# Kernel optimization log

Hardware: AMD Instinct MI355X
Metric: run time of the kernel (lower is better)

## Reference

```python
import jax, jax.numpy as jnp
import numpy as np

# dims: batch, seq, d_model, heads, head_dim, ffn, layers, vocab, group_size
B, S, D, H, DH, DFF, L, V, GS = 2, 1024, 1024, 16, 64, 4096, 2, 32000, 128
EPS = 1e-6


def _dequant(t, s):
    # t: int8 ternary codes [out, in]; s: per-group scales [out*in//GS]
    return (t.reshape(-1, GS).astype(jnp.float32) * s[:, None]).reshape(t.shape)


def _rmsnorm(x, w):
    return x * jax.lax.rsqrt(jnp.mean(x * x, axis=-1, keepdims=True) + EPS) * w


def setup_inputs() -> dict:
    key = jax.random.key(0)
    ks = iter(jax.random.split(key, 64))

    def tern(shape):
        return jax.random.randint(next(ks), shape, -1, 2).astype(jnp.int8)

    def sc(n):
        return jax.random.uniform(next(ks), (n,), minval=0.01, maxval=0.05, dtype=jnp.float32)

    ng_dd = D * D // GS
    ng_fd = DFF * D // GS
    ng_vd = V * D // GS
    inp = {
        'input_ids': jax.random.randint(next(ks), (B, S), 0, V, dtype=jnp.int32),
        'emb_t': tern((V, D)), 'emb_s': sc(ng_vd),
        'qt': tern((L, D, D)), 'qs': jnp.stack([sc(ng_dd) for _ in range(L)]),
        'kt': tern((L, D, D)), 'ks_': jnp.stack([sc(ng_dd) for _ in range(L)]),
        'vt': tern((L, D, D)), 'vs': jnp.stack([sc(ng_dd) for _ in range(L)]),
        'ot': tern((L, D, D)), 'os_': jnp.stack([sc(ng_dd) for _ in range(L)]),
        'gatet': tern((L, DFF, D)), 'gates': jnp.stack([sc(ng_fd) for _ in range(L)]),
        'upt': tern((L, DFF, D)), 'ups': jnp.stack([sc(ng_fd) for _ in range(L)]),
        'downt': tern((L, D, DFF)), 'downs': jnp.stack([sc(ng_fd) for _ in range(L)]),
        'wa': jnp.ones((L, D), jnp.float32),
        'wm': jnp.ones((L, D), jnp.float32),
        'alpha': jnp.full((L, H, 1, 1), 0.5, jnp.float32),
        'wf': jnp.ones((D,), jnp.float32),
        'headt': tern((V, D)), 'heads_': sc(ng_vd),
    }
    return inp


def reference(input_ids, emb_t, emb_s, qt, qs, kt, ks_, vt, vs, ot, os_,
              gatet, gates, upt, ups, downt, downs, wa, wm, alpha, wf,
              headt, heads_):
    # ternary embedding: dequant full table then gather (matches F.embedding on reconstructed weight)
    x = _dequant(emb_t, emb_s)[input_ids]                 # [B, S, D]
    causal = jnp.tril(jnp.ones((S, S), bool))             # [S, S]
    scale = DH ** -0.5
    for l in range(L):
        # --- attention block ---
        h = _rmsnorm(x, wa[l])
        Wq, Wk, Wv, Wo = (_dequant(qt[l], qs[l]), _dequant(kt[l], ks_[l]),
                          _dequant(vt[l], vs[l]), _dequant(ot[l], os_[l]))
        q = (h @ Wq.T).reshape(B, S, H, DH).transpose(0, 2, 1, 3)
        k = (h @ Wk.T).reshape(B, S, H, DH).transpose(0, 2, 1, 3)
        v = (h @ Wv.T).reshape(B, S, H, DH).transpose(0, 2, 1, 3)
        attn = jnp.einsum('bhsd,bhtd->bhst', q, k) * scale
        attn = jnp.where(causal, attn, -jnp.inf)
        p = jax.nn.softmax(attn, axis=-1)
        o = jnp.einsum('bhst,bhtd->bhsd', p, v)
        # per-head residual: alpha * input heads (input to attention is the normed h)
        h_heads = h.reshape(B, S, H, DH).transpose(0, 2, 1, 3)
        o = o + alpha[l] * h_heads
        o = o.transpose(0, 2, 1, 3).reshape(B, S, D)
        x = x + o @ Wo.T
        # --- SwiGLU MLP block ---
        hm = _rmsnorm(x, wm[l])
        Wg, Wu, Wd = (_dequant(gatet[l], gates[l]), _dequant(upt[l], ups[l]),
                      _dequant(downt[l], downs[l]))
        x = x + (jax.nn.silu(hm @ Wg.T) * (hm @ Wu.T)) @ Wd.T
    x = _rmsnorm(x, wf)
    logits = x @ _dequant(headt, heads_).T                # [B, S, V]
    return logits
```

## Files before the change

### kernel.cpp

```cpp
#include <hip/hip_runtime.h>
#include <math.h>
#include <stdint.h>

#define BB   2
#define SS   1024
#define DD   1024
#define HH   16
#define DHH  64
#define DFFD 4096
#define LL   2
#define VV   32000
#define GSZ  128
#define BSR  (BB*SS)
constexpr float EPS = 1e-6f;

typedef unsigned short ushort_t;
typedef __bf16 bf16x8 __attribute__((ext_vector_type(8)));
typedef short  short8 __attribute__((ext_vector_type(8)));
typedef unsigned short ushort8v __attribute__((ext_vector_type(8)));
typedef float  f32x4  __attribute__((ext_vector_type(4)));

__device__ inline ushort_t f2bf(float f) {
    unsigned int u = __builtin_bit_cast(unsigned int, f);
    unsigned int r = u + 0x7fffu + ((u >> 16) & 1u);
    return (ushort_t)(r >> 16);
}
__device__ inline float bf2f(ushort_t u) {
    unsigned int x = ((unsigned int)u) << 16;
    return __builtin_bit_cast(float, x);
}

#define GL2L(g, l) __builtin_amdgcn_global_load_lds( \
    (const __attribute__((address_space(1))) void*)(g), \
    (__attribute__((address_space(3))) void*)(l), 16, 0, 0)

__global__ __launch_bounds__(256) void k_dequant(const int* __restrict__ T,
                                                 const float* __restrict__ S,
                                                 ushort_t* __restrict__ W) {
    int i = (blockIdx.x * 256 + threadIdx.x) * 4;
    int4 t = *(const int4*)(T + i);
    float s = S[i >> 7];
    ushort4 w;
    w.x = f2bf((float)t.x * s); w.y = f2bf((float)t.y * s);
    w.z = f2bf((float)t.z * s); w.w = f2bf((float)t.w * s);
    *(ushort4*)(W + i) = w;
}

__global__ __launch_bounds__(256) void k_embed(const int* __restrict__ ids,
                                               const int* __restrict__ t,
                                               const float* __restrict__ s,
                                               float* __restrict__ x) {
    int row = blockIdx.x;
    int id  = ids[row];
    for (int d = threadIdx.x; d < DD; d += 256) {
        x[(size_t)row * DD + d] =
            (float)t[(size_t)id * DD + d] * s[id * (DD / GSZ) + (d >> 7)];
    }
}

__global__ __launch_bounds__(256) void k_rmsnorm(const float* __restrict__ x,
                                                 const float* __restrict__ w,
                                                 ushort_t* __restrict__ o) {
    int row = blockIdx.x;
    const float* xr = x + (size_t)row * DD;
    float ss = 0.f;
    for (int d = threadIdx.x; d < DD; d += 256) { float v = xr[d]; ss += v * v; }
    __shared__ float sm[4];
    for (int off = 32; off > 0; off >>= 1) ss += __shfl_down(ss, off, 64);
    if ((threadIdx.x & 63) == 0) sm[threadIdx.x >> 6] = ss;
    __syncthreads();
    float tot = sm[0] + sm[1] + sm[2] + sm[3];
    float inv = rsqrtf(tot / DD + EPS);
    for (int d = threadIdx.x; d < DD; d += 256)
        o[(size_t)row * DD + d] = f2bf(xr[d] * inv * w[d]);
}

template <int MODE>
__global__ __launch_bounds__(256) void gemm_bf16(const ushort_t* __restrict__ A,
                                                 const ushort_t* __restrict__ W,
                                                 float* __restrict__ Cf,
                                                 ushort_t* __restrict__ Cb,
                                                 const float* __restrict__ Gf,
                                                 int M, int N, int K) {
    __shared__ ushort_t As[128 * 32];
    __shared__ ushort_t Bs[128 * 32];
    const int tid  = threadIdx.x;
    const int wave = tid >> 6, lane = tid & 63;
    const int wm = wave >> 1, wn = wave & 1;
    const int i0 = blockIdx.y * 128, o0 = blockIdx.x * 128;

    f32x4 acc[4][4] = {};

    const int srow = wave * 32 + (lane >> 2);
    const int scol = (lane & 3) * 8;
    const ushort_t* aG0 = A + (size_t)(i0 + srow) * K + scol;
    const ushort_t* aG1 = aG0 + (size_t)16 * K;
    const ushort_t* bG0 = W + (size_t)(o0 + srow) * K + scol;
    const ushort_t* bG1 = bG0 + (size_t)16 * K;
    ushort_t* aL0 = As + wave * 1024;
    ushort_t* aL1 = aL0 + 512;
    ushort_t* bL0 = Bs + wave * 1024;
    ushort_t* bL1 = bL0 + 512;

    const ushort_t* ap = As + (wm * 64 + (lane & 15)) * 32 + (lane >> 4) * 8;
    const ushort_t* bp = Bs + (wn * 64 + (lane & 15)) * 32 + (lane >> 4) * 8;

    for (int k0 = 0; k0 < K; k0 += 32) {
        __syncthreads();
        GL2L(aG0 + k0, aL0);
        GL2L(aG1 + k0, aL1);
        GL2L(bG0 + k0, bL0);
        GL2L(bG1 + k0, bL1);
        __syncthreads();
        bf16x8 av[4], bv[4];
#pragma unroll
        for (int t = 0; t < 4; ++t) {
            av[t] = __builtin_bit_cast(bf16x8, *(const short8*)(ap + t * 512));
            bv[t] = __builtin_bit_cast(bf16x8, *(const short8*)(bp + t * 512));
        }
#pragma unroll
        for (int mt = 0; mt < 4; ++mt)
#pragma unroll
            for (int nt = 0; nt < 4; ++nt)
                acc[mt][nt] = __builtin_amdgcn_mfma_f32_16x16x32_bf16(
                    av[mt], bv[nt], acc[mt][nt], 0, 0, 0);
    }

    const int r0 = wm * 64 + (lane >> 4) * 4;
    const int c0 = wn * 64 + (lane & 15);
#pragma unroll
    for (int mt = 0; mt < 4; ++mt) {
#pragma unroll
        for (int r = 0; r < 4; ++r) {
            const size_t row = i0 + r0 + mt * 16 + r;
#pragma unroll
            for (int nt = 0; nt < 4; ++nt) {
                const size_t col = o0 + c0 + nt * 16;
                const size_t idx = row * (size_t)N + col;
                float v = acc[mt][nt][r];
                if (MODE == 0) {
                    Cf[idx] = v;
                } else if (MODE == 1) {
                    Cf[idx] += v;
                } else if (MODE == 2) {
                    float gv = Gf[idx];
                    Cb[idx] = f2bf(gv / (1.f + __expf(-gv)) * v);
                } else {
                    Cb[idx] = f2bf(v);
                }
            }
        }
    }
}

__global__ __launch_bounds__(256) void k_fattn(const ushort_t* __restrict__ qkv,
                                               const ushort_t* __restrict__ hn,
                                               const float* __restrict__ alpha,
                                               ushort_t* __restrict__ out) {
    __shared__ ushort_t Ks[64][72];
    __shared__ ushort_t Vt[64][72];
    __shared__ ushort_t Ps[4][16][72];

    const int bid = blockIdx.x;
    const int bh  = bid & 31;
    const int qt  = 15 - (bid >> 5);
    const int hh  = bh & 15;
    const int b   = bh >> 4;
    const int tid = threadIdx.x;
    const int wm  = tid >> 6;
    const int ln  = tid & 63;
    const int m16 = ln & 15;
    const int q4  = ln >> 4;

    const int bS0 = b * SS;
    const int q0  = qt * 64 + wm * 16;

    bf16x8 qa0, qa1;
    {
        const ushort_t* qp = qkv + (size_t)(bS0 + q0 + m16) * 3072 + hh * DHH + q4 * 8;
        qa0 = __builtin_bit_cast(bf16x8, *(const ushort8v*)(qp));
        qa1 = __builtin_bit_cast(bf16x8, *(const ushort8v*)(qp + 32));
    }

    f32x4 oacc[4] = {};
    float mrow[4] = {-1e30f, -1e30f, -1e30f, -1e30f};
    float lrow[4] = {0.f, 0.f, 0.f, 0.f};

    const int c0a = tid, c1a = tid + 256;
    const int r0a = c0a >> 3, cc0 = (c0a & 7) * 8;
    const int r1a = c1a >> 3, cc1 = (c1a & 7) * 8;

    for (int t = 0; t <= qt; ++t) {
        __syncthreads();
        {
            const size_t kbase = (size_t)(bS0 + t * 64) * 3072 + 1024 + hh * DHH;
            *(ushort8v*)&Ks[r0a][cc0] = *(const ushort8v*)(qkv + kbase + (size_t)r0a * 3072 + cc0);
            *(ushort8v*)&Ks[r1a][cc1] = *(const ushort8v*)(qkv + kbase + (size_t)r1a * 3072 + cc1);
            const size_t vbase = (size_t)(bS0 + t * 64) * 3072 + 2048 + hh * DHH;
            ushort8v v0 = *(const ushort8v*)(qkv + vbase + (size_t)r0a * 3072 + cc0);
#pragma unroll
            for (int j = 0; j < 8; ++j) Vt[cc0 + j][r0a] = v0[j];
            ushort8v v1 = *(const ushort8v*)(qkv + vbase + (size_t)r1a * 3072 + cc1);
#pragma unroll
            for (int j = 0; j < 8; ++j) Vt[cc1 + j][r1a] = v1[j];
        }
        __syncthreads();

        f32x4 sc[4];
#pragma unroll
        for (int nt = 0; nt < 4; ++nt) {
            bf16x8 kb0 = __builtin_bit_cast(bf16x8, *(const ushort8v*)&Ks[nt * 16 + m16][q4 * 8]);
            bf16x8 kb1 = __builtin_bit_cast(bf16x8, *(const ushort8v*)&Ks[nt * 16 + m16][32 + q4 * 8]);
            f32x4 z = {};
            z = __builtin_amdgcn_mfma_f32_16x16x32_bf16(qa0, kb0, z, 0, 0, 0);
            sc[nt] = __builtin_amdgcn_mfma_f32_16x16x32_bf16(qa1, kb1, z, 0, 0, 0);
        }

        const bool diag = (t == qt);
#pragma unroll
        for (int r = 0; r < 4; ++r) {
            float s0 = sc[0][r] * 0.125f;
            float s1 = sc[1][r] * 0.125f;
            float s2 = sc[2][r] * 0.125f;
            float s3 = sc[3][r] * 0.125f;
            if (diag) {
                const int rl = wm * 16 + q4 * 4 + r;
                if (m16      > rl) s0 = -1e30f;
                if (m16 + 16 > rl) s1 = -1e30f;
                if (m16 + 32 > rl) s2 = -1e30f;
                if (m16 + 48 > rl) s3 = -1e30f;
            }
            float tm = fmaxf(fmaxf(s0, s1), fmaxf(s2, s3));
            tm = fmaxf(tm, __shfl_xor(tm, 1, 64));
            tm = fmaxf(tm, __shfl_xor(tm, 2, 64));
            tm = fmaxf(tm, __shfl_xor(tm, 4, 64));
            tm = fmaxf(tm, __shfl_xor(tm, 8, 64));
            const float mnew = fmaxf(mrow[r], tm);
            const float corr = __expf(mrow[r] - mnew);
            const float e0 = __expf(s0 - mnew);
            const float e1 = __expf(s1 - mnew);
            const float e2 = __expf(s2 - mnew);
            const float e3 = __expf(s3 - mnew);
            float rs = e0 + e1 + e2 + e3;
            rs += __shfl_xor(rs, 1, 64);
            rs += __shfl_xor(rs, 2, 64);
            rs += __shfl_xor(rs, 4, 64);
            rs += __shfl_xor(rs, 8, 64);
            lrow[r] = lrow[r] * corr + rs;
            mrow[r] = mnew;
#pragma unroll
            for (int dt = 0; dt < 4; ++dt) oacc[dt][r] *= corr;
            const int pr = q4 * 4 + r;
            Ps[wm][pr][m16]      = f2bf(e0);
            Ps[wm][pr][m16 + 16] = f2bf(e1);
            Ps[wm][pr][m16 + 32] = f2bf(e2);
            Ps[wm][pr][m16 + 48] = f2bf(e3);
        }

#pragma unroll
        for (int ks = 0; ks < 2; ++ks) {
            bf16x8 pa = __builtin_bit_cast(bf16x8, *(const ushort8v*)&Ps[wm][m16][ks * 32 + q4 * 8]);
#pragma unroll
            for (int dt = 0; dt < 4; ++dt) {
                bf16x8 vb = __builtin_bit_cast(bf16x8, *(const ushort8v*)&Vt[dt * 16 + m16][ks * 32 + q4 * 8]);
                oacc[dt] = __builtin_amdgcn_mfma_f32_16x16x32_bf16(pa, vb, oacc[dt], 0, 0, 0);
            }
        }
    }

    const float al = alpha[hh];
#pragma unroll
    for (int r = 0; r < 4; ++r) {
        const float inv = 1.f / lrow[r];
        const size_t row = (size_t)(bS0 + q0 + q4 * 4 + r);
#pragma unroll
        for (int dt = 0; dt < 4; ++dt) {
            const size_t idx = row * DD + hh * DHH + dt * 16 + m16;
            out[idx] = f2bf(oacc[dt][r] * inv + al * bf2f(hn[idx]));
        }
    }
}

extern "C" void kernel_launch(void* const* d_in, const int* in_sizes, int n_in,
                              void* d_out, int out_size, void* d_ws, size_t ws_size,
                              hipStream_t stream) {
    const int*   ids   = (const int*)d_in[0];
    const int*   emb_t = (const int*)d_in[1];
    const float* emb_s = (const float*)d_in[2];
    const int*   qt    = (const int*)d_in[3];
    const float* qs    = (const float*)d_in[4];
    const int*   kt    = (const int*)d_in[5];
    const float* ks    = (const float*)d_in[6];
    const int*   vt    = (const int*)d_in[7];
    const float* vs    = (const float*)d_in[8];
    const int*   ot    = (const int*)d_in[9];
    const float* os    = (const float*)d_in[10];
    const int*   gatet = (const int*)d_in[11];
    const float* gates = (const float*)d_in[12];
    const int*   upt   = (const int*)d_in[13];
    const float* ups   = (const float*)d_in[14];
    const int*   downt = (const int*)d_in[15];
    const float* downs = (const float*)d_in[16];
    const float* wa    = (const float*)d_in[17];
    const float* wm    = (const float*)d_in[18];
    const float* alpha = (const float*)d_in[19];
    const float* wf    = (const float*)d_in[20];
    const int*   headt = (const int*)d_in[21];
    const float* heads = (const float*)d_in[22];

    const size_t MB = 1ull << 20;
    char* wsb = (char*)d_ws;
    ushort_t* wbuf = (ushort_t*)(wsb);
    float*    g    = (float*)   (wsb + 24 * MB);
    ushort_t* gb   = (ushort_t*)(wsb + 58 * MB);
    float*    x    = (float*)   (wsb + 75 * MB);
    ushort_t* h    = (ushort_t*)(wsb + 84 * MB);
    ushort_t* qkvb = (ushort_t*)(wsb + 89 * MB);
    ushort_t* ao   = (ushort_t*)(wsb + 102 * MB);

    const size_t wDD = (size_t)DD * DD;
    const size_t sDD = wDD / GSZ;
    const size_t wFD = (size_t)DFFD * DD;
    const size_t sFD = wFD / GSZ;

    k_embed<<<BSR, 256, 0, stream>>>(ids, emb_t, emb_s, x);

    const dim3 gQKV(3072 / 128, BSR / 128);
    const dim3 gD(DD / 128, BSR / 128);
    const dim3 gF(DFFD / 128, BSR / 128);
    const dim3 gV(VV / 128, BSR / 128);

    for (int l = 0; l < LL; ++l) {
        k_rmsnorm<<<BSR, 256, 0, stream>>>(x, wa + l * DD, h);
        k_dequant<<<wDD / 1024, 256, 0, stream>>>(qt + l * wDD, qs + l * sDD, wbuf);
        k_dequant<<<wDD / 1024, 256, 0, stream>>>(kt + l * wDD, ks + l * sDD, wbuf + wDD);
        k_dequant<<<wDD / 1024, 256, 0, stream>>>(vt + l * wDD, vs + l * sDD, wbuf + 2 * wDD);
        gemm_bf16<3><<<gQKV, 256, 0, stream>>>(h, wbuf, nullptr, qkvb, nullptr, BSR, 3072, DD);
        k_fattn<<<16 * BB * HH, 256, 0, stream>>>(qkvb, h, alpha + l * HH, ao);
        k_dequant<<<wDD / 1024, 256, 0, stream>>>(ot + l * wDD, os + l * sDD, wbuf);
        gemm_bf16<1><<<gD, 256, 0, stream>>>(ao, wbuf, x, nullptr, nullptr, BSR, DD, DD);

        k_rmsnorm<<<BSR, 256, 0, stream>>>(x, wm + l * DD, h);
        k_dequant<<<wFD / 1024, 256, 0, stream>>>(gatet + l * wFD, gates + l * sFD, wbuf);
        gemm_bf16<0><<<gF, 256, 0, stream>>>(h, wbuf, g, nullptr, nullptr, BSR, DFFD, DD);
        k_dequant<<<wFD / 1024, 256, 0, stream>>>(upt + l * wFD, ups + l * sFD, wbuf);
        gemm_bf16<2><<<gF, 256, 0, stream>>>(h, wbuf, nullptr, gb, g, BSR, DFFD, DD);
        k_dequant<<<wFD / 1024, 256, 0, stream>>>(downt + l * wFD, downs + l * sFD, wbuf);
        gemm_bf16<1><<<gD, 256, 0, stream>>>(gb, wbuf, x, nullptr, nullptr, BSR, DD, DFFD);
    }

    k_rmsnorm<<<BSR, 256, 0, stream>>>(x, wf, h);
    k_dequant<<<((size_t)VV * DD) / 1024, 256, 0, stream>>>(headt, heads, wbuf);
    gemm_bf16<0><<<gV, 256, 0, stream>>>(h, wbuf, (float*)d_out, nullptr, nullptr, BSR, VV, DD);
}
```

Before: 1.255 ms.

## Fuse gate/up GEMMs via interleaved weights and remap workgroups for XCD locality

Gate and up weights are dequantized into a row-interleaved buffer so that a single GEMM with N=8192 computes both. Adjacent output columns are paired with a lane shuffle and the SwiGLU is applied in the epilogue. This removes the fp32 gate intermediate buffer, one GEMM launch, and the re-read of the activations. All GEMMs also move to a 1D grid with a workgroup remap that groups consecutive blocks on the same XCD, meant to improve L2 reuse. The remap hardcodes 16 M-tiles and needs the block count to be divisible by 8.

Result: faster. 1.217 ms (-3.0%).

```diff
diff --git a/kernel.cpp b/kernel.cpp
--- a/kernel.cpp
+++ b/kernel.cpp
@@ -44,6 +44,20 @@
     w.x = f2bf((float)t.x * s); w.y = f2bf((float)t.y * s);
     w.z = f2bf((float)t.z * s); w.w = f2bf((float)t.w * s);
     *(ushort4*)(W + i) = w;
+}
+
+__global__ __launch_bounds__(256) void k_dequant_il(const int* __restrict__ T,
+                                                    const float* __restrict__ S,
+                                                    ushort_t* __restrict__ W,
+                                                    int which) {
+    int i = (blockIdx.x * 256 + threadIdx.x) * 4;
+    int4 t = *(const int4*)(T + i);
+    float s = S[i >> 7];
+    ushort4 w;
+    w.x = f2bf((float)t.x * s); w.y = f2bf((float)t.y * s);
+    w.z = f2bf((float)t.z * s); w.w = f2bf((float)t.w * s);
+    int r = i >> 10, c = i & 1023;
+    *(ushort4*)(W + (((size_t)((r << 1) | which)) << 10) + c) = w;
 }
 
 __global__ __launch_bounds__(256) void k_embed(const int* __restrict__ ids,
@@ -80,14 +94,18 @@
                                                  const ushort_t* __restrict__ W,
                                                  float* __restrict__ Cf,
                                                  ushort_t* __restrict__ Cb,
-                                                 const float* __restrict__ Gf,
                                                  int M, int N, int K) {
     __shared__ ushort_t As[128 * 32];
     __shared__ ushort_t Bs[128 * 32];
     const int tid  = threadIdx.x;
     const int wave = tid >> 6, lane = tid & 63;
     const int wm = wave >> 1, wn = wave & 1;
-    const int i0 = blockIdx.y * 128, o0 = blockIdx.x * 128;
+
+    const int nwg  = gridDim.x;
+    const int orig = blockIdx.x;
+    const int wgid = (orig & 7) * (nwg >> 3) + (orig >> 3);
+    const int i0 = (wgid & 15) * 128;
+    const int o0 = (wgid >> 4) * 128;
 
     f32x4 acc[4][4] = {};
 
@@ -142,11 +160,15 @@
                     Cf[idx] = v;
                 } else if (MODE == 1) {
                     Cf[idx] += v;
-                } else if (MODE == 2) {
-                    float gv = Gf[idx];
-                    Cb[idx] = f2bf(gv / (1.f + __expf(-gv)) * v);
+                } else if (MODE == 3) {
+                    Cb[idx] = f2bf(v);
                 } else {
-                    Cb[idx] = f2bf(v);
+                    float pv = __shfl_xor(v, 1, 64);
+                    if (!(lane & 1)) {
+                        float g = v, u = pv;
+                        float res = g / (1.f + __expf(-g)) * u;
+                        Cb[row * (size_t)(N >> 1) + (col >> 1)] = f2bf(res);
+                    }
                 }
             }
         }
@@ -311,7 +333,6 @@
     const size_t MB = 1ull << 20;
     char* wsb = (char*)d_ws;
     ushort_t* wbuf = (ushort_t*)(wsb);
-    float*    g    = (float*)   (wsb + 24 * MB);
     ushort_t* gb   = (ushort_t*)(wsb + 58 * MB);
     float*    x    = (float*)   (wsb + 75 * MB);
     ushort_t* h    = (ushort_t*)(wsb + 84 * MB);
@@ -325,31 +346,25 @@
 
     k_embed<<<BSR, 256, 0, stream>>>(ids, emb_t, emb_s, x);
 
-    const dim3 gQKV(3072 / 128, BSR / 128);
-    const dim3 gD(DD / 128, BSR / 128);
-    const dim3 gF(DFFD / 128, BSR / 128);
-    const dim3 gV(VV / 128, BSR / 128);
-
     for (int l = 0; l < LL; ++l) {
         k_rmsnorm<<<BSR, 256, 0, stream>>>(x, wa + l * DD, h);
         k_dequant<<<wDD / 1024, 256, 0, stream>>>(qt + l * wDD, qs + l * sDD, wbuf);
         k_dequant<<<wDD / 1024, 256, 0, stream>>>(kt + l * wDD, ks + l * sDD, wbuf + wDD);
         k_dequant<<<wDD / 1024, 256, 0, stream>>>(vt + l * wDD, vs + l * sDD, wbuf + 2 * wDD);
-        gemm_bf16<3><<<gQKV, 256, 0, stream>>>(h, wbuf, nullptr, qkvb, nullptr, BSR, 3072, DD);
+        gemm_bf16<3><<<24 * 16, 256, 0, stream>>>(h, wbuf, nullptr, qkvb, BSR, 3072, DD);
         k_fattn<<<16 * BB * HH, 256, 0, stream>>>(qkvb, h, alpha + l * HH, ao);
         k_dequant<<<wDD / 1024, 256, 0, stream>>>(ot + l * wDD, os + l * sDD, wbuf);
-        gemm_bf16<1><<<gD, 256, 0, stream>>>(ao, wbuf, x, nullptr, nullptr, BSR, DD, DD);
+        gemm_bf16<1><<<8 * 16, 256, 0, stream>>>(ao, wbuf, x, nullptr, BSR, DD, DD);
 
         k_rmsnorm<<<BSR, 256, 0, stream>>>(x, wm + l * DD, h);
-        k_dequant<<<wFD / 1024, 256, 0, stream>>>(gatet + l * wFD, gates + l * sFD, wbuf);
-        gemm_bf16<0><<<gF, 256, 0, stream>>>(h, wbuf, g, nullptr, nullptr, BSR, DFFD, DD);
-        k_dequant<<<wFD / 1024, 256, 0, stream>>>(upt + l * wFD, ups + l * sFD, wbuf);
-        gemm_bf16<2><<<gF, 256, 0, stream>>>(h, wbuf, nullptr, gb, g, BSR, DFFD, DD);
+        k_dequant_il<<<wFD / 1024, 256, 0, stream>>>(gatet + l * wFD, gates + l * sFD, wbuf, 0);
+        k_dequant_il<<<wFD / 1024, 256, 0, stream>>>(upt + l * wFD, ups + l * sFD, wbuf, 1);
+        gemm_bf16<4><<<64 * 16, 256, 0, stream>>>(h, wbuf, nullptr, gb, BSR, 8192, DD);
         k_dequant<<<wFD / 1024, 256, 0, stream>>>(downt + l * wFD, downs + l * sFD, wbuf);
-        gemm_bf16<1><<<gD, 256, 0, stream>>>(gb, wbuf, x, nullptr, nullptr, BSR, DD, DFFD);
+        gemm_bf16<1><<<8 * 16, 256, 0, stream>>>(gb, wbuf, x, nullptr, BSR, DD, DFFD);
     }
 
     k_rmsnorm<<<BSR, 256, 0, stream>>>(x, wf, h);
     k_dequant<<<((size_t)VV * DD) / 1024, 256, 0, stream>>>(headt, heads, wbuf);
-    gemm_bf16<0><<<gV, 256, 0, stream>>>(h, wbuf, (float*)d_out, nullptr, nullptr, BSR, VV, DD);
-}
+    gemm_bf16<0><<<250 * 16, 256, 0, stream>>>(h, wbuf, (float*)d_out, nullptr, BSR, VV, DD);
+}
```
